# Kernel optimization log

Hardware: AMD Instinct MI355X
Metric: run time of the kernel (lower is better)

## Reference

```python
import jax, jax.numpy as jnp
import numpy as np

N, IN, OUT = 8192, 4096, 4096
GROUP = 4
ACT_BITS = 8


def setup_inputs() -> dict:
    key = jax.random.key(0)
    k_x, k_w, k_b = jax.random.split(key, 3)
    input = jax.random.normal(k_x, (N, IN), dtype=jnp.float32)
    # ternary weights in {-1, 0, +1}, stored as float for compute
    weight = jax.random.randint(k_w, (OUT, IN), -1, 2).astype(jnp.float32)
    weight_scale = jnp.ones((1,), dtype=jnp.float32) * 0.02
    bias = jax.random.normal(k_b, (OUT,), dtype=jnp.float32) * 0.01
    return {"input": input, "weight": weight, "weight_scale": weight_scale, "bias": bias}


def reference(input, weight, weight_scale, bias):
    n, in_f = input.shape
    out_f = weight.shape[0]
    qmax = 2 ** (ACT_BITS - 1) - 1  # 127
    # absmax activation quantization (inference path)
    act_scale = jnp.abs(input).max() / qmax
    x_q = jnp.clip(jnp.round(input / act_scale), -(qmax + 1), qmax)
    # LUT path math: per 4-wide group, contribution = sum(w_group) * mean(x_group)
    g = in_f // GROUP
    x_mean = x_q.reshape(n, g, GROUP).mean(axis=-1)          # [N, G]
    w_sum = weight.reshape(out_f, g, GROUP).sum(axis=-1)     # [OUT, G]
    out = jnp.einsum('ng,og->no', x_mean, w_sum)
    out = out * weight_scale * act_scale + bias
    return out
```

## Files before the change

kernel.cpp:

```cpp
#include <hip/hip_runtime.h>

#define NROWS 8192
#define INF   4096
#define OUTF  4096
#define G     1024

typedef _Float16 f16x8 __attribute__((ext_vector_type(8)));
typedef float    f32x4 __attribute__((ext_vector_type(4)));


__global__ void pass1(const float4* __restrict__ x,
                      const float4* __restrict__ w,
                      float* __restrict__ partial,
                      _Float16* __restrict__ ws) {
    const int t = threadIdx.x;
    const int b = blockIdx.x;
    if (b < 2048) {
        const int stride = 2048 * 256;
        int i = b * 256 + t;
        float m = 0.f;
        #pragma unroll 4
        for (int it = 0; it < 16; ++it, i += stride) {
            float4 v = x[i];
            m = fmaxf(m, fmaxf(fmaxf(fabsf(v.x), fabsf(v.y)),
                               fmaxf(fabsf(v.z), fabsf(v.w))));
        }
        for (int off = 32; off; off >>= 1)
            m = fmaxf(m, __shfl_down(m, off));
        __shared__ float wm[4];
        int lane = t & 63, wave = t >> 6;
        if (lane == 0) wm[wave] = m;
        __syncthreads();
        if (t == 0)
            partial[b] = fmaxf(fmaxf(wm[0], wm[1]), fmaxf(wm[2], wm[3]));
    } else {
        int i = (b - 2048) * 4096 + t;
        #pragma unroll 4
        for (int it = 0; it < 16; ++it, i += 256) {
            float4 v = w[i];
            ws[i] = (_Float16)(v.x + v.y + v.z + v.w);
        }
    }
}

__global__ void absmax_final(const float* __restrict__ partial,
                             const float* __restrict__ wscale,
                             float* __restrict__ sc) {
    int t = threadIdx.x;
    float m = 0.f;
    #pragma unroll
    for (int u = 0; u < 8; ++u)
        m = fmaxf(m, partial[t + u * 256]);
    for (int off = 32; off; off >>= 1)
        m = fmaxf(m, __shfl_down(m, off));
    __shared__ float wm[4];
    int lane = t & 63, wave = t >> 6;
    if (lane == 0) wm[wave] = m;
    __syncthreads();
    if (t == 0) {
        float bm = fmaxf(fmaxf(wm[0], wm[1]), fmaxf(wm[2], wm[3]));
        float s = bm * (1.0f / 127.0f);
        sc[0] = s;
        sc[1] = 127.0f / bm;
        sc[2] = s * 0.25f * wscale[0];
    }
}

__global__ void xquant(const float4* __restrict__ x,
                       const float* __restrict__ sc,
                       _Float16* __restrict__ xs) {
    const float inv = sc[1];
    int i0 = blockIdx.x * 512 + threadIdx.x;
    #pragma unroll
    for (int u = 0; u < 2; ++u) {
        int i = i0 + u * 256;
        float4 v = x[i];
        xs[i] = (_Float16)(rintf(v.x * inv) + rintf(v.y * inv) +
                           rintf(v.z * inv) + rintf(v.w * inv));
    }
}

#define BM 256
#define BN 128
#define BK 32

__device__ __forceinline__ void async_copy16(const void* g, void* l) {
    __builtin_amdgcn_global_load_lds(
        (const __attribute__((address_space(1))) unsigned int*)g,
        (__attribute__((address_space(3))) unsigned int*)l,
        16, 0, 0);
}

__global__ __launch_bounds__(256, 2) void gemm_kernel(
    const _Float16* __restrict__ A,
    const _Float16* __restrict__ B,
    const float* __restrict__ bias,
    const float* __restrict__ sc,
    float* __restrict__ out) {

    __shared__ alignas(16) _Float16 As[2][BM * BK];
    __shared__ alignas(16) _Float16 Bs[2][BN * BK];

    const int t = threadIdx.x;
    const int lane = t & 63;
    const int wave = t >> 6;
    const int wm = (wave >> 1) * 128;
    const int wn = (wave & 1) * 64;

    const long rowA0 = (long)blockIdx.y * BM;
    const long rowB0 = (long)blockIdx.x * BN;

    f32x4 acc[8][4] = {};

    const int srow = lane >> 2;
    const int scol = ((lane & 3) << 3) ^ (((lane >> 3) & 3) << 3);
    const int swzR = ((lane >> 1) & 3) << 3;

    auto stage = [&](int buf, int k0) {
        #pragma unroll
        for (int i = 0; i < 6; ++i) {
            const int c = wave * 6 + i;
            if (c < 16) {
                const int row = c * 16 + srow;
                async_copy16(A + (rowA0 + row) * (long)G + k0 + scol, &As[buf][c * 512]);
            } else {
                const int row = (c - 16) * 16 + srow;
                async_copy16(B + (rowB0 + row) * (long)G + k0 + scol, &Bs[buf][(c - 16) * 512]);
            }
        }
    };

    stage(0, 0);
    __syncthreads();

    int cur = 0;
    for (int ks = 0; ks < G / BK; ++ks) {
        if (ks + 1 < G / BK) stage(cur ^ 1, (ks + 1) * BK);

        f16x8 af[8], bf[4];
        #pragma unroll
        for (int mi = 0; mi < 8; ++mi)
            af[mi] = *(const f16x8*)&As[cur][(wm + mi * 16 + (lane & 15)) * BK
                                            + (((lane >> 4) * 8) ^ swzR)];
        #pragma unroll
        for (int nj = 0; nj < 4; ++nj)
            bf[nj] = *(const f16x8*)&Bs[cur][(wn + nj * 16 + (lane & 15)) * BK
                                            + (((lane >> 4) * 8) ^ swzR)];

        #pragma unroll
        for (int mi = 0; mi < 8; ++mi)
            #pragma unroll
            for (int nj = 0; nj < 4; ++nj)
                acc[mi][nj] = __builtin_amdgcn_mfma_f32_16x16x32_f16(
                    af[mi], bf[nj], acc[mi][nj], 0, 0, 0);

        __syncthreads();
        cur ^= 1;
    }

    const float scale = sc[2];
    const int r0 = (int)rowA0 + wm + (lane >> 4) * 4;
    const int c0 = (int)rowB0 + wn + (lane & 15);
    #pragma unroll
    for (int nj = 0; nj < 4; ++nj) {
        const int col = c0 + nj * 16;
        const float b = bias[col];
        #pragma unroll
        for (int mi = 0; mi < 8; ++mi) {
            const int row = r0 + mi * 16;
            #pragma unroll
            for (int r = 0; r < 4; ++r)
                out[(long)(row + r) * OUTF + col] = acc[mi][nj][r] * scale + b;
        }
    }
}

extern "C" void kernel_launch(void* const* d_in, const int* in_sizes, int n_in,
                              void* d_out, int out_size, void* d_ws, size_t ws_size,
                              hipStream_t stream) {
    const float* input  = (const float*)d_in[0];
    const float* weight = (const float*)d_in[1];
    const float* wscale = (const float*)d_in[2];
    const float* bias   = (const float*)d_in[3];
    float* out = (float*)d_out;

    float* scales   = (float*)d_ws;
    float* partials = (float*)((char*)d_ws + 16);
    _Float16* x_sum = (_Float16*)((char*)d_ws + 8208);
    _Float16* w_sum = (_Float16*)((char*)d_ws + 8208 + (size_t)NROWS * G * 2);

    pass1<<<3072, 256, 0, stream>>>((const float4*)input, (const float4*)weight,
                                    partials, w_sum);
    absmax_final<<<1, 256, 0, stream>>>(partials, wscale, scales);
    xquant<<<16384, 256, 0, stream>>>((const float4*)input, scales, x_sum);
    gemm_kernel<<<dim3(OUTF / BN, NROWS / BM), 256, 0, stream>>>(
        x_sum, w_sum, bias, scales, out);
}
```

Measured before the change: 386.5 us.

## Triple-buffer GEMM pipeline, swizzle block order, fuse absmax finalize into xquant

The GEMM moves from double to triple buffering of the LDS tiles. It waits with explicit vmcnt counts and raw barriers, so loads run two stages ahead. Blocks are remapped so that groups of 8 consecutive blocks cover different row tiles, which is meant to improve L2 reuse. The separate absmax_final launch is removed: every xquant block recomputes the final max from the partials, with fewer and larger blocks. Nontemporal loads are used for the weights and nontemporal stores for the output, which adds LDS pressure and relies on the hand-set vmcnt values being correct.

```diff
diff --git a/kernel.cpp b/kernel.cpp
--- a/kernel.cpp
+++ b/kernel.cpp
@@ -7,6 +7,7 @@
 
 typedef _Float16 f16x8 __attribute__((ext_vector_type(8)));
 typedef float    f32x4 __attribute__((ext_vector_type(4)));
+typedef float    f32x4v __attribute__((ext_vector_type(4)));
 
 
 __global__ void pass1(const float4* __restrict__ x,
@@ -37,16 +38,18 @@
         int i = (b - 2048) * 4096 + t;
         #pragma unroll 4
         for (int it = 0; it < 16; ++it, i += 256) {
-            float4 v = w[i];
+            f32x4v v = __builtin_nontemporal_load((const f32x4v*)&w[i]);
             ws[i] = (_Float16)(v.x + v.y + v.z + v.w);
         }
     }
 }
 
-__global__ void absmax_final(const float* __restrict__ partial,
-                             const float* __restrict__ wscale,
-                             float* __restrict__ sc) {
-    int t = threadIdx.x;
+__global__ void xquant(const float4* __restrict__ x,
+                       const float* __restrict__ partial,
+                       const float* __restrict__ wscale,
+                       float* __restrict__ sc,
+                       _Float16* __restrict__ xs) {
+    const int t = threadIdx.x;
     float m = 0.f;
     #pragma unroll
     for (int u = 0; u < 8; ++u)
@@ -57,23 +60,16 @@
     int lane = t & 63, wave = t >> 6;
     if (lane == 0) wm[wave] = m;
     __syncthreads();
-    if (t == 0) {
-        float bm = fmaxf(fmaxf(wm[0], wm[1]), fmaxf(wm[2], wm[3]));
+    const float bm = fmaxf(fmaxf(wm[0], wm[1]), fmaxf(wm[2], wm[3]));
+    const float inv = 127.0f / bm;
+    if (blockIdx.x == 0 && t == 0) {
         float s = bm * (1.0f / 127.0f);
         sc[0] = s;
-        sc[1] = 127.0f / bm;
         sc[2] = s * 0.25f * wscale[0];
     }
-}
-
-__global__ void xquant(const float4* __restrict__ x,
-                       const float* __restrict__ sc,
-                       _Float16* __restrict__ xs) {
-    const float inv = sc[1];
-    int i0 = blockIdx.x * 512 + threadIdx.x;
-    #pragma unroll
-    for (int u = 0; u < 2; ++u) {
-        int i = i0 + u * 256;
+    int i = blockIdx.x * 4096 + t;
+    #pragma unroll 4
+    for (int it = 0; it < 16; ++it, i += 256) {
         float4 v = x[i];
         xs[i] = (_Float16)(rintf(v.x * inv) + rintf(v.y * inv) +
                            rintf(v.z * inv) + rintf(v.w * inv));
@@ -83,6 +79,7 @@
 #define BM 256
 #define BN 128
 #define BK 32
+#define NT (G / BK)
 
 __device__ __forceinline__ void async_copy16(const void* g, void* l) {
     __builtin_amdgcn_global_load_lds(
@@ -98,8 +95,8 @@
     const float* __restrict__ sc,
     float* __restrict__ out) {
 
-    __shared__ alignas(16) _Float16 As[2][BM * BK];
-    __shared__ alignas(16) _Float16 Bs[2][BN * BK];
+    __shared__ alignas(16) _Float16 As[3][BM * BK];
+    __shared__ alignas(16) _Float16 Bs[3][BN * BK];
 
     const int t = threadIdx.x;
     const int lane = t & 63;
@@ -107,8 +104,13 @@
     const int wm = (wave >> 1) * 128;
     const int wn = (wave & 1) * 64;
 
-    const long rowA0 = (long)blockIdx.y * BM;
-    const long rowB0 = (long)blockIdx.x * BN;
+    const int lin = blockIdx.y * gridDim.x + blockIdx.x;
+    const int swz = (lin & 7) * 128 + (lin >> 3);
+    const int bx = swz & 31;
+    const int by = swz >> 5;
+
+    const long rowA0 = (long)by * BM;
+    const long rowB0 = (long)bx * BN;
 
     f32x4 acc[8][4] = {};
 
@@ -116,7 +118,8 @@
     const int scol = ((lane & 3) << 3) ^ (((lane >> 3) & 3) << 3);
     const int swzR = ((lane >> 1) & 3) << 3;
 
-    auto stage = [&](int buf, int k0) {
+    auto stage = [&](int buf, int kt) {
+        const int k0 = kt * BK;
         #pragma unroll
         for (int i = 0; i < 6; ++i) {
             const int c = wave * 6 + i;
@@ -131,21 +134,28 @@
     };
 
     stage(0, 0);
-    __syncthreads();
-
-    int cur = 0;
-    for (int ks = 0; ks < G / BK; ++ks) {
-        if (ks + 1 < G / BK) stage(cur ^ 1, (ks + 1) * BK);
+    stage(1, 1);
+
+    int rb = 0;
+    for (int ks = 0; ks < NT; ++ks) {
+        if (ks + 2 < NT) {
+            int sb = rb + 2; if (sb >= 3) sb -= 3;
+            stage(sb, ks + 2);
+        }
+        if (ks < NT - 2)       asm volatile("s_waitcnt vmcnt(12)" ::: "memory");
+        else if (ks == NT - 2) asm volatile("s_waitcnt vmcnt(6)" ::: "memory");
+        else                   asm volatile("s_waitcnt vmcnt(0)" ::: "memory");
+        __builtin_amdgcn_s_barrier();
 
         f16x8 af[8], bf[4];
         #pragma unroll
         for (int mi = 0; mi < 8; ++mi)
-            af[mi] = *(const f16x8*)&As[cur][(wm + mi * 16 + (lane & 15)) * BK
-                                            + (((lane >> 4) * 8) ^ swzR)];
+            af[mi] = *(const f16x8*)&As[rb][(wm + mi * 16 + (lane & 15)) * BK
+                                           + (((lane >> 4) * 8) ^ swzR)];
         #pragma unroll
         for (int nj = 0; nj < 4; ++nj)
-            bf[nj] = *(const f16x8*)&Bs[cur][(wn + nj * 16 + (lane & 15)) * BK
-                                            + (((lane >> 4) * 8) ^ swzR)];
+            bf[nj] = *(const f16x8*)&Bs[rb][(wn + nj * 16 + (lane & 15)) * BK
+                                           + (((lane >> 4) * 8) ^ swzR)];
 
         #pragma unroll
         for (int mi = 0; mi < 8; ++mi)
@@ -154,8 +164,8 @@
                 acc[mi][nj] = __builtin_amdgcn_mfma_f32_16x16x32_f16(
                     af[mi], bf[nj], acc[mi][nj], 0, 0, 0);
 
-        __syncthreads();
-        cur ^= 1;
+        __builtin_amdgcn_s_barrier();
+        ++rb; if (rb == 3) rb = 0;
     }
 
     const float scale = sc[2];
@@ -170,7 +180,8 @@
             const int row = r0 + mi * 16;
             #pragma unroll
             for (int r = 0; r < 4; ++r)
-                out[(long)(row + r) * OUTF + col] = acc[mi][nj][r] * scale + b;
+                __builtin_nontemporal_store(acc[mi][nj][r] * scale + b,
+                                            &out[(long)(row + r) * OUTF + col]);
         }
     }
 }
@@ -191,8 +202,8 @@
 
     pass1<<<3072, 256, 0, stream>>>((const float4*)input, (const float4*)weight,
                                     partials, w_sum);
-    absmax_final<<<1, 256, 0, stream>>>(partials, wscale, scales);
-    xquant<<<16384, 256, 0, stream>>>((const float4*)input, scales, x_sum);
+    xquant<<<2048, 256, 0, stream>>>((const float4*)input, partials, wscale,
+                                     scales, x_sum);
     gemm_kernel<<<dim3(OUTF / BN, NROWS / BM), 256, 0, stream>>>(
         x_sum, w_sum, bias, scales, out);
 }
```

New measurement: 374.7 us. 1.03x faster.

## Fuse prep kernels via cooperative grid sync and enlarge GEMM tile

Applied to the files above, without the earlier changes.

Merges the absmax partial pass, the weight group-sum, the final absmax reduction and the activation quantization into one cooperative kernel that uses a grid-wide sync instead of three separate launches. The weight read is marked nontemporal. The GEMM moves to 256x256 tiles with BK=64 and 512 threads, a new XOR swizzle, and explicit vmcnt waits with raw barriers so the next stage's loads overlap the current compute. The goal is fewer launches and better operand reuse, at the cost of depending on cooperative launch residency and carrying more LDS and register pressure per block.

```diff
diff --git a/kernel.cpp b/kernel.cpp
--- a/kernel.cpp
+++ b/kernel.cpp
@@ -1,4 +1,7 @@
 #include <hip/hip_runtime.h>
+#include <hip/hip_cooperative_groups.h>
+
+namespace cg = cooperative_groups;
 
 #define NROWS 8192
 #define INF   4096
@@ -9,80 +12,77 @@
 typedef float    f32x4 __attribute__((ext_vector_type(4)));
 
 
-__global__ void pass1(const float4* __restrict__ x,
-                      const float4* __restrict__ w,
-                      float* __restrict__ partial,
-                      _Float16* __restrict__ ws) {
+__global__ __launch_bounds__(256, 4) void prep(
+    const float4* __restrict__ x,
+    const float4* __restrict__ w,
+    const float* __restrict__ wscale,
+    float* __restrict__ partial,
+    float* __restrict__ sc,
+    _Float16* __restrict__ xs,
+    _Float16* __restrict__ ws) {
+
     const int t = threadIdx.x;
     const int b = blockIdx.x;
-    if (b < 2048) {
-        const int stride = 2048 * 256;
-        int i = b * 256 + t;
+    const int tid = b * 256 + t;
+    const int stride = 1024 * 256;
+    const int lane = t & 63, wave = t >> 6;
+    __shared__ float wm[4];
+
+    {
         float m = 0.f;
+        int i = tid;
         #pragma unroll 4
-        for (int it = 0; it < 16; ++it, i += stride) {
+        for (int it = 0; it < 32; ++it, i += stride) {
             float4 v = x[i];
             m = fmaxf(m, fmaxf(fmaxf(fabsf(v.x), fabsf(v.y)),
                                fmaxf(fabsf(v.z), fabsf(v.w))));
         }
         for (int off = 32; off; off >>= 1)
             m = fmaxf(m, __shfl_down(m, off));
-        __shared__ float wm[4];
-        int lane = t & 63, wave = t >> 6;
         if (lane == 0) wm[wave] = m;
         __syncthreads();
         if (t == 0)
             partial[b] = fmaxf(fmaxf(wm[0], wm[1]), fmaxf(wm[2], wm[3]));
-    } else {
-        int i = (b - 2048) * 4096 + t;
+    }
+    {
+        int i = tid;
         #pragma unroll 4
-        for (int it = 0; it < 16; ++it, i += 256) {
-            float4 v = w[i];
+        for (int it = 0; it < 16; ++it, i += stride) {
+            f32x4 v = __builtin_nontemporal_load((const f32x4*)&w[i]);
             ws[i] = (_Float16)(v.x + v.y + v.z + v.w);
         }
     }
-}
-
-__global__ void absmax_final(const float* __restrict__ partial,
-                             const float* __restrict__ wscale,
-                             float* __restrict__ sc) {
-    int t = threadIdx.x;
-    float m = 0.f;
-    #pragma unroll
-    for (int u = 0; u < 8; ++u)
-        m = fmaxf(m, partial[t + u * 256]);
-    for (int off = 32; off; off >>= 1)
-        m = fmaxf(m, __shfl_down(m, off));
-    __shared__ float wm[4];
-    int lane = t & 63, wave = t >> 6;
-    if (lane == 0) wm[wave] = m;
-    __syncthreads();
-    if (t == 0) {
-        float bm = fmaxf(fmaxf(wm[0], wm[1]), fmaxf(wm[2], wm[3]));
-        float s = bm * (1.0f / 127.0f);
-        sc[0] = s;
-        sc[1] = 127.0f / bm;
-        sc[2] = s * 0.25f * wscale[0];
-    }
-}
-
-__global__ void xquant(const float4* __restrict__ x,
-                       const float* __restrict__ sc,
-                       _Float16* __restrict__ xs) {
-    const float inv = sc[1];
-    int i0 = blockIdx.x * 512 + threadIdx.x;
-    #pragma unroll
-    for (int u = 0; u < 2; ++u) {
-        int i = i0 + u * 256;
-        float4 v = x[i];
-        xs[i] = (_Float16)(rintf(v.x * inv) + rintf(v.y * inv) +
-                           rintf(v.z * inv) + rintf(v.w * inv));
+    __threadfence();
+    cg::this_grid().sync();
+
+    {
+        float m = fmaxf(fmaxf(partial[t], partial[t + 256]),
+                        fmaxf(partial[t + 512], partial[t + 768]));
+        for (int off = 32; off; off >>= 1)
+            m = fmaxf(m, __shfl_down(m, off));
+        if (lane == 0) wm[wave] = m;
+        __syncthreads();
+        const float bm = fmaxf(fmaxf(wm[0], wm[1]), fmaxf(wm[2], wm[3]));
+        const float inv = 127.0f / bm;
+        if (b == 0 && t == 0) {
+            float s = bm * (1.0f / 127.0f);
+            sc[0] = s;
+            sc[2] = s * 0.25f * wscale[0];
+        }
+        int i = tid;
+        #pragma unroll 4
+        for (int it = 0; it < 32; ++it, i += stride) {
+            float4 v = x[i];
+            xs[i] = (_Float16)(rintf(v.x * inv) + rintf(v.y * inv) +
+                               rintf(v.z * inv) + rintf(v.w * inv));
+        }
     }
 }
 
 #define BM 256
-#define BN 128
-#define BK 32
+#define BN 256
+#define BK 64
+#define KSTEPS (G / BK)
 
 __device__ __forceinline__ void async_copy16(const void* g, void* l) {
     __builtin_amdgcn_global_load_lds(
@@ -91,7 +91,7 @@
         16, 0, 0);
 }
 
-__global__ __launch_bounds__(256, 2) void gemm_kernel(
+__global__ __launch_bounds__(512, 2) void gemm_kernel(
     const _Float16* __restrict__ A,
     const _Float16* __restrict__ B,
     const float* __restrict__ bias,
@@ -104,63 +104,76 @@
     const int t = threadIdx.x;
     const int lane = t & 63;
     const int wave = t >> 6;
-    const int wm = (wave >> 1) * 128;
-    const int wn = (wave & 1) * 64;
+    const int wm = (wave >> 2) * 128;
+    const int wn = (wave & 3) * 64;
 
     const long rowA0 = (long)blockIdx.y * BM;
     const long rowB0 = (long)blockIdx.x * BN;
 
     f32x4 acc[8][4] = {};
 
-    const int srow = lane >> 2;
-    const int scol = ((lane & 3) << 3) ^ (((lane >> 3) & 3) << 3);
-    const int swzR = ((lane >> 1) & 3) << 3;
-
-    auto stage = [&](int buf, int k0) {
+    const int srow = lane >> 3;
+    const int scolB = ((lane & 7) ^ srow) << 4;
+
+    auto stage = [&](int buf, int kt) {
+        const long kbyte = (long)kt * (BK * 2);
         #pragma unroll
-        for (int i = 0; i < 6; ++i) {
-            const int c = wave * 6 + i;
-            if (c < 16) {
-                const int row = c * 16 + srow;
-                async_copy16(A + (rowA0 + row) * (long)G + k0 + scol, &As[buf][c * 512]);
+        for (int i = 0; i < 8; ++i) {
+            const int c = wave * 8 + i;
+            if (c < 32) {
+                const long row = c * 8 + srow;
+                async_copy16((const char*)A + (rowA0 + row) * (G * 2) + kbyte + scolB,
+                             (char*)&As[buf][0] + c * 1024);
             } else {
-                const int row = (c - 16) * 16 + srow;
-                async_copy16(B + (rowB0 + row) * (long)G + k0 + scol, &Bs[buf][(c - 16) * 512]);
+                const long row = (c - 32) * 8 + srow;
+                async_copy16((const char*)B + (rowB0 + row) * (G * 2) + kbyte + scolB,
+                             (char*)&Bs[buf][0] + (c - 32) * 1024);
             }
         }
     };
 
+    const int fr = lane & 15;
+    const int fq16 = (lane >> 4) << 4;
+    const int fswz = (lane & 7) << 4;
+
     stage(0, 0);
-    __syncthreads();
-
-    int cur = 0;
-    for (int ks = 0; ks < G / BK; ++ks) {
-        if (ks + 1 < G / BK) stage(cur ^ 1, (ks + 1) * BK);
-
-        f16x8 af[8], bf[4];
+    int buf = 0;
+    for (int ks = 0; ks < KSTEPS; ++ks) {
+        if (ks + 1 < KSTEPS) {
+            stage(buf ^ 1, ks + 1);
+            asm volatile("s_waitcnt vmcnt(8)" ::: "memory");
+        } else {
+            asm volatile("s_waitcnt vmcnt(0)" ::: "memory");
+        }
+        __builtin_amdgcn_s_barrier();
+
         #pragma unroll
-        for (int mi = 0; mi < 8; ++mi)
-            af[mi] = *(const f16x8*)&As[cur][(wm + mi * 16 + (lane & 15)) * BK
-                                            + (((lane >> 4) * 8) ^ swzR)];
-        #pragma unroll
-        for (int nj = 0; nj < 4; ++nj)
-            bf[nj] = *(const f16x8*)&Bs[cur][(wn + nj * 16 + (lane & 15)) * BK
-                                            + (((lane >> 4) * 8) ^ swzR)];
-
-        #pragma unroll
-        for (int mi = 0; mi < 8; ++mi)
+        for (int kh = 0; kh < 2; ++kh) {
+            const int cb = kh * 64;
+            f16x8 af[8], bf[4];
+            #pragma unroll
+            for (int mi = 0; mi < 8; ++mi)
+                af[mi] = *(const f16x8*)((const char*)&As[buf][0]
+                           + (wm + mi * 16 + fr) * 128 + ((cb + fq16) ^ fswz));
             #pragma unroll
             for (int nj = 0; nj < 4; ++nj)
-                acc[mi][nj] = __builtin_amdgcn_mfma_f32_16x16x32_f16(
-                    af[mi], bf[nj], acc[mi][nj], 0, 0, 0);
-
-        __syncthreads();
-        cur ^= 1;
+                bf[nj] = *(const f16x8*)((const char*)&Bs[buf][0]
+                           + (wn + nj * 16 + fr) * 128 + ((cb + fq16) ^ fswz));
+            #pragma unroll
+            for (int mi = 0; mi < 8; ++mi)
+                #pragma unroll
+                for (int nj = 0; nj < 4; ++nj)
+                    acc[mi][nj] = __builtin_amdgcn_mfma_f32_16x16x32_f16(
+                        af[mi], bf[nj], acc[mi][nj], 0, 0, 0);
+        }
+
+        __builtin_amdgcn_s_barrier();
+        buf ^= 1;
     }
 
     const float scale = sc[2];
     const int r0 = (int)rowA0 + wm + (lane >> 4) * 4;
-    const int c0 = (int)rowB0 + wn + (lane & 15);
+    const int c0 = (int)rowB0 + wn + fr;
     #pragma unroll
     for (int nj = 0; nj < 4; ++nj) {
         const int col = c0 + nj * 16;
@@ -178,10 +191,10 @@
 extern "C" void kernel_launch(void* const* d_in, const int* in_sizes, int n_in,
                               void* d_out, int out_size, void* d_ws, size_t ws_size,
                               hipStream_t stream) {
-    const float* input  = (const float*)d_in[0];
-    const float* weight = (const float*)d_in[1];
-    const float* wscale = (const float*)d_in[2];
-    const float* bias   = (const float*)d_in[3];
+    const float4* input  = (const float4*)d_in[0];
+    const float4* weight = (const float4*)d_in[1];
+    const float* wscale  = (const float*)d_in[2];
+    const float* bias    = (const float*)d_in[3];
     float* out = (float*)d_out;
 
     float* scales   = (float*)d_ws;
@@ -189,10 +202,10 @@
     _Float16* x_sum = (_Float16*)((char*)d_ws + 8208);
     _Float16* w_sum = (_Float16*)((char*)d_ws + 8208 + (size_t)NROWS * G * 2);
 
-    pass1<<<3072, 256, 0, stream>>>((const float4*)input, (const float4*)weight,
-                                    partials, w_sum);
-    absmax_final<<<1, 256, 0, stream>>>(partials, wscale, scales);
-    xquant<<<16384, 256, 0, stream>>>((const float4*)input, scales, x_sum);
-    gemm_kernel<<<dim3(OUTF / BN, NROWS / BM), 256, 0, stream>>>(
+    void* args[] = {(void*)&input, (void*)&weight, (void*)&wscale, (void*)&partials,
+                    (void*)&scales, (void*)&x_sum, (void*)&w_sum};
+    hipLaunchCooperativeKernel((void*)prep, dim3(1024), dim3(256), args, 0, stream);
+
+    gemm_kernel<<<dim3(OUTF / BN, NROWS / BM), 512, 0, stream>>>(
         x_sum, w_sum, bias, scales, out);
 }
```

Measured after the change: 628.9 us. 1.63x slower.
